# Kernel tuning notes

Hardware: AMD Instinct MI355X
Metric: run time of the kernel (lower is better)

## Reference

```python
import jax, jax.numpy as jnp
import numpy as np

LN_EPS = 1e-5
L1_EPS = 1e-12  # F.normalize clamp_min eps


def _layernorm(h, g, b):
    mu = h.mean(-1, keepdims=True)
    var = ((h - mu) ** 2).mean(-1, keepdims=True)
    return (h - mu) * jax.lax.rsqrt(var + LN_EPS) * g + b


def _graph(x, wq_w, wq_b, wk_w, wk_b, gcn_w, ln_g, ln_b):
    # x: [..., n, d]
    qx = x @ wq_w.T + wq_b
    kx = x @ wk_w.T + wk_b
    dot = jnp.einsum('...nd,...md->...nm', qx, kx)
    sq = dot * dot
    adj = sq / jnp.maximum(sq.sum(-1, keepdims=True), L1_EPS)  # L1-normalized rows
    for i in range(gcn_w.shape[0]):
        h = adj @ (x @ gcn_w[i])
        x = jax.nn.relu(_layernorm(h, ln_g[i], ln_b[i]))
    return x.mean(-2)  # mean over nodes -> [..., d]


def setup_inputs() -> dict:
    key = jax.random.key(0)
    ks = jax.random.split(key, 12)
    N, FR, B, NF = 16, 32, 50, 768
    L, NC = 2, 400
    s = 1.0 / np.sqrt(NF)
    inp = {
        'feats': jax.random.normal(ks[0], (N, FR, B, NF), jnp.float32),
        'feat_global_single': jax.random.normal(ks[1], (N, NF), jnp.float32),
        'feat_single_previous': jax.random.normal(ks[2], (N, NF), jnp.float32),
        'wq_w': jax.random.normal(ks[3], (NF, NF), jnp.float32) * s,
        'wq_b': jnp.zeros((NF,), jnp.float32),
        'wk_w': jax.random.normal(ks[4], (NF, NF), jnp.float32) * s,
        'wk_b': jnp.zeros((NF,), jnp.float32),
        'gcn_w': jax.random.normal(ks[5], (L, NF, NF), jnp.float32) * s,
        'ln_g': jnp.ones((L, NF), jnp.float32),
        'ln_b': jnp.zeros((L, NF), jnp.float32),
        'fc1_w': jax.random.normal(ks[6], (NF, 2 * NF), jnp.float32) / np.sqrt(2 * NF),
        'fc1_b': jnp.zeros((NF,), jnp.float32),
        'fc2_w': jax.random.normal(ks[7], (NC, NF), jnp.float32) * s,
        'fc2_b': jnp.zeros((NC,), jnp.float32),
        't_c': 0,
    }
    return inp


def reference(feats, feat_global_single, feat_single_previous,
              wq_w, wq_b, wk_w, wk_b, gcn_w, ln_g, ln_b,
              fc1_w, fc1_b, fc2_w, fc2_b, t_c):
    N, FR, B, NF = feats.shape
    x = feats.reshape(N * FR, B, NF)
    # object-level graph (shared weights)
    x = _graph(x, wq_w, wq_b, wk_w, wk_b, gcn_w, ln_g, ln_b)  # [N*FR, NF]
    x = x.reshape(N, FR, NF)
    # frame-level graph (same shared weights)
    x = _graph(x, wq_w, wq_b, wk_w, wk_b, gcn_w, ln_g, ln_b)  # [N, NF]
    y = jnp.concatenate([x, feat_global_single], axis=-1)      # [N, 2*NF]
    # ClassifierSimple (dropout = identity in eval)
    h = jax.nn.relu(y @ fc1_w.T + fc1_b)
    logits = h @ fc2_w.T + fc2_b
    return (logits, y)
```

## Files before the change

kernel.cpp:

```cpp
#include <hip/hip_runtime.h>
#include <hip/hip_bf16.h>

typedef unsigned short u16;
typedef unsigned int   u32;
typedef __attribute__((ext_vector_type(8))) short short8;
typedef __attribute__((ext_vector_type(4))) float float4v;

__device__ __forceinline__ float bf2f(u16 u){ union{u32 i; float f;} c; c.i = ((u32)u) << 16; return c.f; }
__device__ __forceinline__ float bflo(u32 u){ union{u32 i; float f;} c; c.i = u << 16; return c.f; }
__device__ __forceinline__ float bfhi(u32 u){ union{u32 i; float f;} c; c.i = u & 0xFFFF0000u; return c.f; }
__device__ __forceinline__ u16 f2bf(float f){
  union{float f; u32 i;} c; c.f = f; u32 x = c.i;
  return (u16)((x + 0x7FFFu + ((x >> 16) & 1u)) >> 16);
}
__device__ __forceinline__ u32 pack2(float a, float b){
  union { __hip_bfloat162 h; u32 u; } c;
  c.h = __float22bfloat162_rn(float2{a, b});
  return c.u;
}

__device__ __forceinline__ void async16(const void* g, void* l){
  __builtin_amdgcn_global_load_lds((const __attribute__((address_space(1))) void*)g,
                                   (__attribute__((address_space(3))) void*)l, 16, 0, 0);
}

__global__ void prep_w(const float* __restrict__ wq, const float* __restrict__ wk,
                       const float* __restrict__ gcn,
                       u16* __restrict__ WqT, u16* __restrict__ WkT,
                       u16* __restrict__ QHB768, u16* __restrict__ gcnT1)
{
  __shared__ float tile[32][33];
  int z = blockIdx.z;
  const float* src = (z == 0) ? wq : (z == 1) ? wk : gcn + (size_t)(z - 2) * 589824;
  u16* dst = (z == 0) ? WqT : (z == 1) ? WkT : (z == 2) ? QHB768 : gcnT1;
  int r0 = blockIdx.y * 32, c0 = blockIdx.x * 32;
  int tx = threadIdx.x, ty = threadIdx.y;
  for (int i = 0; i < 32; i += 8) tile[ty + i][tx] = src[(size_t)(r0 + ty + i) * 768 + c0 + tx];
  __syncthreads();
  for (int i = 0; i < 32; i += 8) dst[(size_t)(c0 + ty + i) * 768 + r0 + tx] = f2bf(tile[tx][ty + i]);
}

__global__ void __launch_bounds__(256) prep_uv2(const float* __restrict__ wq, const float* __restrict__ wk,
                                                const float* __restrict__ wqb, const float* __restrict__ wkb,
                                                float* __restrict__ uv, float* __restrict__ cbuf)
{
  __shared__ float red[4][64];
  __shared__ float r2[256];
  int b = blockIdx.x, tid = threadIdx.x;
  if (b < 24) {
    const float* w  = (b < 12) ? wq : wk;
    const float* bs = (b < 12) ? wkb : wqb;
    int out = (b % 12) * 64 + (tid & 63);
    int oq = tid >> 6;
    float a = 0.f;
    for (int o = oq * 192; o < oq * 192 + 192; o++) a += w[(size_t)o * 768 + out] * bs[o];
    red[oq][tid & 63] = a;
    __syncthreads();
    if (tid < 64)
      uv[((b < 12) ? 0 : 768) + (b % 12) * 64 + tid] = red[0][tid] + red[1][tid] + red[2][tid] + red[3][tid];
  } else {
    float a = 0.f;
    for (int o = tid; o < 768; o += 256) a += wqb[o] * wkb[o];
    r2[tid] = a; __syncthreads();
    if (tid == 0) { float s = 0.f; for (int i = 0; i < 256; i++) s += r2[i]; cbuf[0] = s; }
  }
}

__global__ void __launch_bounds__(256) conv_pq(const float* __restrict__ src, u16* __restrict__ dst,
                                               const float* __restrict__ uv, const float* __restrict__ cbuf,
                                               float* __restrict__ p, float* __restrict__ q)
{
  __shared__ float us[768], vs[768];
  int tid = threadIdx.x, lane = tid & 63;
  for (int i = tid; i < 768; i += 256) { us[i] = uv[i]; vs[i] = uv[768 + i]; }
  __syncthreads();
  size_t rbase = (size_t)blockIdx.x * 8;
  int row = tid >> 5;
  int c3  = (tid & 31) * 3;
  const float* s = src + (rbase + row) * 768 + (size_t)c3 * 8;
  u16* d = dst + (rbase + row) * 768 + (size_t)c3 * 8;
  float ap = 0.f, aq = 0.f;
#pragma unroll
  for (int j = 0; j < 3; j++) {
    float4 a = ((const float4*)s)[j * 2];
    float4 b = ((const float4*)s)[j * 2 + 1];
    uint4 o = { pack2(a.x, a.y), pack2(a.z, a.w), pack2(b.x, b.y), pack2(b.z, b.w) };
    ((uint4*)d)[j] = o;
    const float* uu = &us[(c3 + j) * 8];
    const float* vv = &vs[(c3 + j) * 8];
    ap += a.x*uu[0] + a.y*uu[1] + a.z*uu[2] + a.w*uu[3] + b.x*uu[4] + b.y*uu[5] + b.z*uu[6] + b.w*uu[7];
    aq += a.x*vv[0] + a.y*vv[1] + a.z*vv[2] + a.w*vv[3] + b.x*vv[4] + b.y*vv[5] + b.z*vv[6] + b.w*vv[7];
  }
  for (int m = 1; m <= 16; m <<= 1) { ap += __shfl_xor(ap, m); aq += __shfl_xor(aq, m); }
  if ((lane & 31) == 0) {
    p[rbase + row] = ap + cbuf[0];
    q[rbase + row] = aq;
  }
}

__global__ void __launch_bounds__(256) gemm_bt(const u16* __restrict__ A, const u16* __restrict__ Bw,
                                               const float* __restrict__ bias, u16* __restrict__ C,
                                               int M, int N, int K)
{
  __shared__ __attribute__((aligned(16))) u16 As[128 * 64];
  __shared__ __attribute__((aligned(16))) u16 Bs[128 * 64];
  int tid = threadIdx.x, lane = tid & 63, wid = tid >> 6;
  int wm = wid >> 1, wn = wid & 1;
  size_t m0 = (size_t)blockIdx.x * 128, n0 = (size_t)blockIdx.y * 128;

  float4v acc[4][4];
  for (int r = 0; r < 4; r++) for (int c = 0; c < 4; c++) acc[r][c] = (float4v){0.f, 0.f, 0.f, 0.f};

  int srow8  = lane >> 3;
  int schunk = (lane & 7) ^ srow8;
  const u16* gA[4]; const u16* gB[4];
  u16* lA[4]; u16* lB[4];
#pragma unroll
  for (int j = 0; j < 4; j++) {
    int r = 32 * wid + 8 * j + srow8;
    gA[j] = A  + (m0 + r) * (size_t)K + schunk * 8;
    gB[j] = Bw + (n0 + r) * (size_t)K + schunk * 8;
    lA[j] = &As[(32 * wid + 8 * j) * 64];
    lB[j] = &Bs[(32 * wid + 8 * j) * 64];
  }

  int l15 = lane & 15, quad = lane >> 4;
  int s0 = quad ^ (l15 & 7);

  for (int kt = 0; kt < K; kt += 64) {
#pragma unroll
    for (int j = 0; j < 4; j++) {
      async16(gA[j] + kt, lA[j]);
      async16(gB[j] + kt, lB[j]);
    }
    __syncthreads();
#pragma unroll
    for (int ks = 0; ks < 2; ks++) {
      int so = (s0 ^ (ks << 2)) * 8;
      short8 af[4], bfr[4];
#pragma unroll
      for (int r = 0; r < 4; r++) af[r]  = *(const short8*)&As[(wm * 64 + r * 16 + l15) * 64 + so];
#pragma unroll
      for (int c = 0; c < 4; c++) bfr[c] = *(const short8*)&Bs[(wn * 64 + c * 16 + l15) * 64 + so];
#pragma unroll
      for (int r = 0; r < 4; r++)
#pragma unroll
        for (int c = 0; c < 4; c++)
          acc[r][c] = __builtin_amdgcn_mfma_f32_16x16x32_bf16(af[r], bfr[c], acc[r][c], 0, 0, 0);
    }
    __syncthreads();
  }

  int quad4 = quad * 4;
  for (int c = 0; c < 4; c++) {
    int n = (int)n0 + wn * 64 + c * 16 + l15;
    float bv = bias ? bias[n] : 0.f;
    for (int r = 0; r < 4; r++) {
      size_t mbase = m0 + wm * 64 + r * 16 + quad4;
      for (int t = 0; t < 4; t++)
        C[(mbase + t) * (size_t)N + n] = f2bf(acc[r][c][t] + bv);
    }
  }
}


template<int NP>
__global__ void __launch_bounds__(512) fused_l1(const u16* __restrict__ TH, const u16* __restrict__ AR,
                                                const float* __restrict__ pb, const float* __restrict__ qb,
                                                const float* __restrict__ lng, const float* __restrict__ lnb,
                                                u16* __restrict__ adjG, u16* __restrict__ X, int n, int Mtot)
{
  constexpr int ST = 72;
  constexpr int TPW = (NP == 64) ? 2 : 1;
  constexpr int SR = NP;
  __shared__ __attribute__((aligned(16))) u16 adjb[NP * ST];
  __shared__ __attribute__((aligned(16))) u16 HT[2][64 * ST];
  __shared__ __attribute__((aligned(16))) u16 As1[SR * 64];
  __shared__ __attribute__((aligned(16))) u16 Bs1[SR * 64];
  __shared__ float rsum[NP];
  __shared__ float stats[NP][2];
  __shared__ float bc[NP][2];
  __shared__ float ps[NP], qs[NP];
  __shared__ float lg[768], lb[768];

  int g = blockIdx.x;
  int tid = threadIdx.x, lane = tid & 63, w = tid >> 6;
  int l15 = lane & 15, quad = lane >> 4;

  for (int i = tid; i < 768; i += 512) { lg[i] = lng[i]; lb[i] = lnb[i]; }
  if (tid < NP) {
    rsum[tid] = 0.f; stats[tid][0] = 0.f; stats[tid][1] = 0.f;
    ps[tid] = (tid < n) ? pb[(size_t)g * n + tid] : 0.f;
    qs[tid] = (tid < n) ? qb[(size_t)g * n + tid] : 0.f;
  }
  __syncthreads();

  int mt, nt0; bool s_act;
  if (NP == 64) { mt = w & 3; nt0 = (w >> 2) * 2; s_act = true; }
  else          { mt = w & 1; nt0 = w >> 1;       s_act = (w < 4); }

  int srow8  = lane >> 3;
  int schunk = (lane & 7) ^ srow8;
  int trow   = (NP == 64) ? (8 * w + srow8) : (8 * (w & 3) + srow8);
  size_t grow = (size_t)g * n + trow;
  if (grow >= (size_t)Mtot) grow = Mtot - 1;
  const u16* gA1 = TH + grow * 1536 + schunk * 8;
  const u16* gB1 = AR + grow * 768  + schunk * 8;
  u16* lA1 = &As1[((NP == 64) ? 8 * w : 8 * (w & 3)) * 64];
  u16* lB1 = &Bs1[((NP == 64) ? 8 * w : 8 * (w & 3)) * 64];
  int s0 = quad ^ (l15 & 7);

  float4v sacc[TPW];
  for (int j = 0; j < TPW; j++) sacc[j] = (float4v){0.f, 0.f, 0.f, 0.f};

  for (int kt = 0; kt < 768; kt += 64) {
    if (NP == 64) {
      async16(gA1 + kt, lA1);
      async16(gB1 + kt, lB1);
    } else {
      if (w < 4) async16(gA1 + kt, lA1);
      else       async16(gB1 + kt, lB1);
    }
    __syncthreads();
    if (s_act) {
#pragma unroll
      for (int ks = 0; ks < 2; ks++) {
        int so = (s0 ^ (ks << 2)) * 8;
        short8 a = *(const short8*)&As1[(mt * 16 + l15) * 64 + so];
#pragma unroll
        for (int j = 0; j < TPW; j++) {
          short8 b = *(const short8*)&Bs1[((nt0 + j) * 16 + l15) * 64 + so];
          sacc[j] = __builtin_amdgcn_mfma_f32_16x16x32_bf16(a, b, sacc[j], 0, 0, 0);
        }
      }
    }
    __syncthreads();
  }

  if (s_act) {
    for (int j = 0; j < TPW; j++) {
      int col = (nt0 + j) * 16 + l15;
      bool cok = col < n;
      for (int t = 0; t < 4; t++) {
        int row = mt * 16 + quad * 4 + t;
        sacc[j][t] = cok ? (sacc[j][t] + ps[row] + qs[col]) : 0.f;
      }
    }
    for (int t = 0; t < 4; t++) {
      float s = 0.f;
      for (int j = 0; j < TPW; j++) { float v = sacc[j][t]; s += v * v; }
      s += __shfl_xor(s, 1); s += __shfl_xor(s, 2); s += __shfl_xor(s, 4); s += __shfl_xor(s, 8);
      if (l15 == 0) atomicAdd(&rsum[mt * 16 + quad * 4 + t], s);
    }
  }
  __syncthreads();
  if (tid < NP) rsum[tid] = 1.0f / fmaxf(rsum[tid], 1e-12f);
  __syncthreads();
  if (s_act) {
    u16* gadj = adjG + (size_t)g * NP * NP;
    for (int j = 0; j < TPW; j++)
      for (int t = 0; t < 4; t++) {
        int row = mt * 16 + quad * 4 + t, col = (nt0 + j) * 16 + l15;
        float v = sacc[j][t];
        u16 b = f2bf(v * v * rsum[row]);
        adjb[row * ST + col] = b;
        gadj[row * NP + col] = b;
      }
  }
  __syncthreads();

  int m2, nt20;
  if (NP == 64) { m2 = w & 3; nt20 = (w >> 2) * 2; }
  else          { m2 = w & 1; nt20 = w >> 1; }

  float4v xacc[12][TPW];
#pragma unroll
  for (int ch = 0; ch < 12; ch++) for (int j = 0; j < TPW; j++) xacc[ch][j] = (float4v){0.f,0.f,0.f,0.f};

  int hj  = tid & (NP - 1);
  int hseg= (NP == 64) ? w : ((tid >> 5) & 7);
  bool hact = (NP == 64) ? true : (tid < NP * 8);
  const u16* hbase = TH + ((size_t)g * n + hj) * 1536 + 768 + hseg * 8;

  uint4 hcur = {0,0,0,0};
  if (hact && hj < n) hcur = *(const uint4*)(hbase);

#pragma unroll
  for (int ch = 0; ch < 12; ch++) {
    uint4 hnext = {0,0,0,0};
    if (ch < 11 && hact && hj < n) hnext = *(const uint4*)(hbase + (ch + 1) * 64);
    u16* htb = HT[ch & 1];
    if (hact) {
      const u16* ep = (const u16*)&hcur;
      for (int i = 0; i < 8; i++) htb[(hseg * 8 + i) * ST + hj] = ep[i];
    }
    __syncthreads();
    for (int k = 0; k < NP / 32; k++) {
      short8 a = *(const short8*)&adjb[(m2 * 16 + l15) * ST + k * 32 + quad * 8];
      for (int j = 0; j < TPW; j++) {
        short8 b = *(const short8*)&htb[((nt20 + j) * 16 + l15) * ST + k * 32 + quad * 8];
        xacc[ch][j] = __builtin_amdgcn_mfma_f32_16x16x32_bf16(a, b, xacc[ch][j], 0, 0, 0);
      }
    }
    hcur = hnext;
  }

  float ssum[4] = {0,0,0,0}, ssq[4] = {0,0,0,0};
#pragma unroll
  for (int ch = 0; ch < 12; ch++)
    for (int j = 0; j < TPW; j++)
      for (int t = 0; t < 4; t++) { float v = xacc[ch][j][t]; ssum[t] += v; ssq[t] += v * v; }
  for (int m = 1; m <= 8; m <<= 1)
    for (int t = 0; t < 4; t++) { ssum[t] += __shfl_xor(ssum[t], m); ssq[t] += __shfl_xor(ssq[t], m); }
  if (l15 == 0)
    for (int t = 0; t < 4; t++) {
      atomicAdd(&stats[m2 * 16 + quad * 4 + t][0], ssum[t]);
      atomicAdd(&stats[m2 * 16 + quad * 4 + t][1], ssq[t]);
    }
  __syncthreads();
  if (tid < NP) {
    float mu = stats[tid][0] * (1.f / 768.f);
    float var = stats[tid][1] * (1.f / 768.f) - mu * mu;
    bc[tid][0] = mu; bc[tid][1] = rsqrtf(fmaxf(var, 0.f) + 1e-5f);
  }
  __syncthreads();

#pragma unroll
  for (int ch = 0; ch < 12; ch++)
    for (int j = 0; j < TPW; j++)
      for (int t = 0; t < 4; t++) {
        int row = m2 * 16 + quad * 4 + t;
        if (row < n) {
          int d = ch * 64 + (nt20 + j) * 16 + l15;
          float v = fmaxf((xacc[ch][j][t] - bc[row][0]) * bc[row][1] * lg[d] + lb[d], 0.f);
          X[((size_t)g * n + row) * 768 + d] = f2bf(v);
        }
      }
}

template<int NP>
__global__ void __launch_bounds__(512) fused_l2(const u16* __restrict__ adjG, const u16* __restrict__ H,
                                                const float* __restrict__ lng, const float* __restrict__ lnb,
                                                u16* __restrict__ Xmean, int n, float inv,
                                                const float* __restrict__ uvg, const float* __restrict__ cbuf,
                                                float* __restrict__ pOut, float* __restrict__ qOut)
{
  constexpr int ST = 72;
  constexpr int TPW = (NP == 64) ? 2 : 1;
  __shared__ __attribute__((aligned(16))) u16 adjb[NP * ST];
  __shared__ __attribute__((aligned(16))) u16 HT[2][64 * ST];
  __shared__ float stats[NP][2];
  __shared__ float bc[NP][2];
  __shared__ float colsum[768];
  __shared__ float lg[768], lb[768];
  __shared__ float pr[8][2];

  int g = blockIdx.x;
  int tid = threadIdx.x, lane = tid & 63, w = tid >> 6;
  int l15 = lane & 15, quad = lane >> 4;

  for (int i = tid; i < 768; i += 512) { lg[i] = lng[i]; lb[i] = lnb[i]; colsum[i] = 0.f; }
  if (tid < NP) { stats[tid][0] = 0.f; stats[tid][1] = 0.f; }
  if (tid * 8 < NP * NP) {
    int row = (tid * 8) / NP, c0 = (tid * 8) % NP;
    uint4 v = *(const uint4*)(adjG + (size_t)g * NP * NP + row * NP + c0);
    *(uint4*)&adjb[row * ST + c0] = v;
  }

  int m2, nt20;
  if (NP == 64) { m2 = w & 3; nt20 = (w >> 2) * 2; }
  else          { m2 = w & 1; nt20 = w >> 1; }

  float4v xacc[12][TPW];
#pragma unroll
  for (int ch = 0; ch < 12; ch++) for (int j = 0; j < TPW; j++) xacc[ch][j] = (float4v){0.f,0.f,0.f,0.f};

  int hj  = tid & (NP - 1);
  int hseg= (NP == 64) ? w : ((tid >> 5) & 7);
  bool hact = (NP == 64) ? true : (tid < NP * 8);
  const u16* hbase = H + ((size_t)g * n + hj) * 768 + hseg * 8;

  uint4 hcur = {0,0,0,0};
  if (hact && hj < n) hcur = *(const uint4*)(hbase);

  __syncthreads();

#pragma unroll
  for (int ch = 0; ch < 12; ch++) {
    uint4 hnext = {0,0,0,0};
    if (ch < 11 && hact && hj < n) hnext = *(const uint4*)(hbase + (ch + 1) * 64);
    u16* htb = HT[ch & 1];
    if (hact) {
      const u16* ep = (const u16*)&hcur;
      for (int i = 0; i < 8; i++) htb[(hseg * 8 + i) * ST + hj] = ep[i];
    }
    __syncthreads();
    for (int k = 0; k < NP / 32; k++) {
      short8 a = *(const short8*)&adjb[(m2 * 16 + l15) * ST + k * 32 + quad * 8];
      for (int j = 0; j < TPW; j++) {
        short8 b = *(const short8*)&htb[((nt20 + j) * 16 + l15) * ST + k * 32 + quad * 8];
        xacc[ch][j] = __builtin_amdgcn_mfma_f32_16x16x32_bf16(a, b, xacc[ch][j], 0, 0, 0);
      }
    }
    hcur = hnext;
  }

  float ssum[4] = {0,0,0,0}, ssq[4] = {0,0,0,0};
#pragma unroll
  for (int ch = 0; ch < 12; ch++)
    for (int j = 0; j < TPW; j++)
      for (int t = 0; t < 4; t++) { float v = xacc[ch][j][t]; ssum[t] += v; ssq[t] += v * v; }
  for (int m = 1; m <= 8; m <<= 1)
    for (int t = 0; t < 4; t++) { ssum[t] += __shfl_xor(ssum[t], m); ssq[t] += __shfl_xor(ssq[t], m); }
  if (l15 == 0)
    for (int t = 0; t < 4; t++) {
      atomicAdd(&stats[m2 * 16 + quad * 4 + t][0], ssum[t]);
      atomicAdd(&stats[m2 * 16 + quad * 4 + t][1], ssq[t]);
    }
  __syncthreads();
  if (tid < NP) {
    float mu = stats[tid][0] * (1.f / 768.f);
    float var = stats[tid][1] * (1.f / 768.f) - mu * mu;
    bc[tid][0] = mu; bc[tid][1] = rsqrtf(fmaxf(var, 0.f) + 1e-5f);
  }
  __syncthreads();

#pragma unroll
  for (int ch = 0; ch < 12; ch++)
    for (int j = 0; j < TPW; j++)
      for (int t = 0; t < 4; t++) {
        int row = m2 * 16 + quad * 4 + t;
        int d = ch * 64 + (nt20 + j) * 16 + l15;
        float v = fmaxf((xacc[ch][j][t] - bc[row][0]) * bc[row][1] * lg[d] + lb[d], 0.f);
        float vm = (row < n) ? v : 0.f;
        vm += __shfl_xor(vm, 16);
        vm += __shfl_xor(vm, 32);
        if (quad == 0) atomicAdd(&colsum[d], vm);
      }
  __syncthreads();
  if (tid < 384)
    ((u32*)Xmean)[(size_t)g * 384 + tid] = pack2(colsum[tid * 2] * inv, colsum[tid * 2 + 1] * inv);

  if (pOut) {
    float pp = 0.f, qq = 0.f;
    if (tid < 384) {
      float x0 = colsum[tid * 2] * inv, x1 = colsum[tid * 2 + 1] * inv;
      pp = x0 * uvg[tid * 2] + x1 * uvg[tid * 2 + 1];
      qq = x0 * uvg[768 + tid * 2] + x1 * uvg[768 + tid * 2 + 1];
    }
    for (int m = 1; m <= 32; m <<= 1) { pp += __shfl_xor(pp, m); qq += __shfl_xor(qq, m); }
    if (lane == 0) { pr[w][0] = pp; pr[w][1] = qq; }
    __syncthreads();
    if (tid == 0) {
      float sp = 0.f, sq = 0.f;
      for (int i = 0; i < 8; i++) { sp += pr[i][0]; sq += pr[i][1]; }
      pOut[g] = sp + cbuf[0]; qOut[g] = sq;
    }
  }
}

__global__ void __launch_bounds__(384) concat_y(const u16* __restrict__ Xm,
                                                const float* __restrict__ fgs, float* __restrict__ yout)
{
  int b = blockIdx.x, tid = threadIdx.x;
  u32 u = ((const u32*)Xm)[(size_t)b * 384 + tid];
  int d0 = tid * 2;
  yout[(size_t)b * 1536 + d0]     = bflo(u);
  yout[(size_t)b * 1536 + d0 + 1] = bfhi(u);
  yout[(size_t)b * 1536 + 768 + d0]     = fgs[(size_t)b * 768 + d0];
  yout[(size_t)b * 1536 + 768 + d0 + 1] = fgs[(size_t)b * 768 + d0 + 1];
}

__global__ void __launch_bounds__(256) fc1_relu(const float* __restrict__ yout,
                                                const float* __restrict__ fc1w, const float* __restrict__ fc1b,
                                                float* __restrict__ h)
{
  int o = blockIdx.x * 4 + (threadIdx.x >> 6);
  int lane = threadIdx.x & 63;
  float acc[16];
  for (int b = 0; b < 16; b++) acc[b] = 0.f;
  const float4* wr = (const float4*)(fc1w + (size_t)o * 1536);
  for (int k4 = lane; k4 < 384; k4 += 64) {
    float4 wv = wr[k4];
    for (int b = 0; b < 16; b++) {
      float4 yv = ((const float4*)(yout + (size_t)b * 1536))[k4];
      acc[b] += wv.x * yv.x + wv.y * yv.y + wv.z * yv.z + wv.w * yv.w;
    }
  }
  for (int m = 1; m <= 32; m <<= 1)
    for (int b = 0; b < 16; b++) acc[b] += __shfl_xor(acc[b], m);
  if (lane < 16) h[(size_t)lane * 768 + o] = fmaxf(acc[lane] + fc1b[o], 0.f);
}

__global__ void __launch_bounds__(256) fc2_out(const float* __restrict__ h,
                                               const float* __restrict__ fc2w, const float* __restrict__ fc2b,
                                               float* __restrict__ logits)
{
  int o = blockIdx.x * 4 + (threadIdx.x >> 6);
  int lane = threadIdx.x & 63;
  float acc[16];
  for (int b = 0; b < 16; b++) acc[b] = 0.f;
  const float4* wr = (const float4*)(fc2w + (size_t)o * 768);
  for (int k4 = lane; k4 < 192; k4 += 64) {
    float4 wv = wr[k4];
    for (int b = 0; b < 16; b++) {
      float4 hv = ((const float4*)(h + (size_t)b * 768))[k4];
      acc[b] += wv.x * hv.x + wv.y * hv.y + wv.z * hv.z + wv.w * hv.w;
    }
  }
  for (int m = 1; m <= 32; m <<= 1)
    for (int b = 0; b < 16; b++) acc[b] += __shfl_xor(acc[b], m);
  if (lane < 16) logits[(size_t)lane * 400 + o] = acc[lane] + fc2b[o];
}

extern "C" void kernel_launch(void* const* d_in, const int* in_sizes, int n_in,
                              void* d_out, int out_size, void* d_ws, size_t ws_size,
                              hipStream_t stream) {
  const float* feats = (const float*)d_in[0];
  const float* fgs   = (const float*)d_in[1];
  const float* wq_w  = (const float*)d_in[3];
  const float* wq_b  = (const float*)d_in[4];
  const float* wk_w  = (const float*)d_in[5];
  const float* wk_b  = (const float*)d_in[6];
  const float* gcn_w = (const float*)d_in[7];
  const float* ln_g  = (const float*)d_in[8];
  const float* ln_b  = (const float*)d_in[9];
  const float* fc1_w = (const float*)d_in[10];
  const float* fc1_b = (const float*)d_in[11];
  const float* fc2_w = (const float*)d_in[12];
  const float* fc2_b = (const float*)d_in[13];
  float* out  = (float*)d_out;
  float* yout = out + 16 * 400;

  char* ws = (char*)d_ws;
  size_t off = 0;
  auto alloc = [&](size_t b){ size_t r = off; off = (off + b + 255) & ~(size_t)255; return r; };
  u16*  QHB    = (u16*) (ws + alloc((size_t)1536 * 768 * 2));
  u16*  gcnT1  = (u16*) (ws + alloc((size_t)768 * 768 * 2));
  u16*  WqT    = (u16*) (ws + alloc((size_t)768 * 768 * 2));
  u16*  WkT    = (u16*) (ws + alloc((size_t)768 * 768 * 2));
  float* uv    = (float*)(ws + alloc((size_t)1536 * 4));
  float* cbuf  = (float*)(ws + alloc((size_t)4));
  u16*  Abf    = (u16*) (ws + alloc((size_t)25600 * 768 * 2));
  float* pObj  = (float*)(ws + alloc((size_t)25600 * 4));
  float* qObj  = (float*)(ws + alloc((size_t)25600 * 4));
  float* pF    = (float*)(ws + alloc((size_t)512 * 4));
  float* qF    = (float*)(ws + alloc((size_t)512 * 4));
  u16*  Xf     = (u16*) (ws + alloc((size_t)512 * 768 * 2));
  u16*  QHf    = (u16*) (ws + alloc((size_t)512 * 1536 * 2));
  u16*  X1f    = (u16*) (ws + alloc((size_t)512 * 768 * 2));
  u16*  H2f    = (u16*) (ws + alloc((size_t)512 * 768 * 2));
  u16*  adjFb  = (u16*) (ws + alloc((size_t)16 * 32 * 32 * 2));
  u16*  Xm     = (u16*) (ws + alloc((size_t)16 * 768 * 2));
  float* hbuf  = (float*)(ws + alloc((size_t)16 * 768 * 4));
  size_t base = off;

  auto need = [&](int GC){
    size_t R = (size_t)GC * 50;
    return base + R * 1536 * 2 + 512 + R * 768 * 2 + 512 + (size_t)GC * 64 * 64 * 2 + 512;
  };
  int GC = 64;
  if (need(512) <= ws_size) GC = 512;
  else if (need(256) <= ws_size) GC = 256;
  else if (need(128) <= ws_size) GC = 128;
  int R = GC * 50;
  size_t off2 = base;
  auto alloc2 = [&](size_t b){ size_t r = off2; off2 = (off2 + b + 255) & ~(size_t)255; return r; };
  u16* QHc   = (u16*)(ws + alloc2((size_t)R * 1536 * 2));
  u16* X1c   = (u16*)(ws + alloc2((size_t)R * 768 * 2));
  u16* adjGc = (u16*)(ws + alloc2((size_t)GC * 64 * 64 * 2));
  u16* H2c   = QHc;

  prep_w<<<dim3(24, 24, 4), dim3(32, 8), 0, stream>>>(wq_w, wk_w, gcn_w, WqT, WkT,
                                                      QHB + (size_t)768 * 768, gcnT1);
  prep_uv2<<<25, 256, 0, stream>>>(wq_w, wk_w, wq_b, wk_b, uv, cbuf);
  gemm_bt<<<dim3(6, 6), 256, 0, stream>>>(WkT, WqT, nullptr, QHB, 768, 768, 768);
  conv_pq<<<3200, 256, 0, stream>>>(feats, Abf, uv, cbuf, pObj, qObj);

  int nchunks = 512 / GC;
  for (int c = 0; c < nchunks; c++) {
    const u16* fc = Abf + (size_t)c * GC * 50 * 768;
    gemm_bt<<<dim3(R / 128, 12), 256, 0, stream>>>(fc, QHB, nullptr, QHc, R, 1536, 768);
    fused_l1<64><<<GC, 512, 0, stream>>>(QHc, fc, pObj + (size_t)c * GC * 50, qObj + (size_t)c * GC * 50,
                                         ln_g, ln_b, adjGc, X1c, 50, R);
    gemm_bt<<<dim3(R / 128, 6), 256, 0, stream>>>(X1c, gcnT1, nullptr, H2c, R, 768, 768);
    fused_l2<64><<<GC, 512, 0, stream>>>(adjGc, H2c, ln_g + 768, ln_b + 768,
                                         Xf + (size_t)c * GC * 768, 50, 1.f / 50.f,
                                         uv, cbuf, pF + (size_t)c * GC, qF + (size_t)c * GC);
  }

  gemm_bt<<<dim3(4, 12), 256, 0, stream>>>(Xf, QHB, nullptr, QHf, 512, 1536, 768);
  fused_l1<32><<<16, 512, 0, stream>>>(QHf, Xf, pF, qF, ln_g, ln_b, adjFb, X1f, 32, 512);
  gemm_bt<<<dim3(4, 6), 256, 0, stream>>>(X1f, gcnT1, nullptr, H2f, 512, 768, 768);
  fused_l2<32><<<16, 512, 0, stream>>>(adjFb, H2f, ln_g + 768, ln_b + 768, Xm, 32, 1.f / 32.f,
                                       uv, cbuf, nullptr, nullptr);

  concat_y<<<16, 384, 0, stream>>>(Xm, fgs, yout);
  fc1_relu<<<192, 256, 0, stream>>>(yout, fc1_w, fc1_b, hbuf);
  fc2_out<<<100, 256, 0, stream>>>(hbuf, fc2_w, fc2_b, out);
}
```

Before: 494.8 us.

## Produce transposed H via swapped GEMM operands and load with swizzled vector LDS stores

The combined QH GEMM is split into two calls. One keeps the row-major T output. The other swaps operands so that H1 and H2 are written transposed (feature-major, leading dimension R). The fused graph kernels then load H with 16-byte vector LDS stores into an XOR-swizzled layout, replacing the 8-way scalar transposing scatter and removing the per-row bounds checks. Padding and a zero_tail kernel cover reads past the last group. In exchange, the transposed GEMM has a different output write pattern and there is an extra launch, and rows read past n pick up neighbouring groups' data, which must be masked by zero adjacency.

```diff
diff --git a/kernel.cpp b/kernel.cpp
--- a/kernel.cpp
+++ b/kernel.cpp
@@ -66,6 +66,12 @@
   }
 }
 
+__global__ void zero_tail(u16* a, u16* b, u16* c, u16* d)
+{
+  int t = threadIdx.x;
+  a[t] = 0; b[t] = 0; c[t] = 0; d[t] = 0;
+}
+
 __global__ void __launch_bounds__(256) conv_pq(const float* __restrict__ src, u16* __restrict__ dst,
                                                const float* __restrict__ uv, const float* __restrict__ cbuf,
                                                float* __restrict__ p, float* __restrict__ q)
@@ -165,18 +171,19 @@
 
 
 template<int NP>
-__global__ void __launch_bounds__(512) fused_l1(const u16* __restrict__ TH, const u16* __restrict__ AR,
+__global__ void __launch_bounds__(512) fused_l1(const u16* __restrict__ Tc, const u16* __restrict__ AR,
                                                 const float* __restrict__ pb, const float* __restrict__ qb,
                                                 const float* __restrict__ lng, const float* __restrict__ lnb,
-                                                u16* __restrict__ adjG, u16* __restrict__ X, int n, int Mtot)
+                                                u16* __restrict__ adjG, u16* __restrict__ X, int n, int Mtot,
+                                                const u16* __restrict__ HTg, int ldH)
 {
   constexpr int ST = 72;
   constexpr int TPW = (NP == 64) ? 2 : 1;
-  constexpr int SR = NP;
+  constexpr int NOCT = NP / 8;
   __shared__ __attribute__((aligned(16))) u16 adjb[NP * ST];
-  __shared__ __attribute__((aligned(16))) u16 HT[2][64 * ST];
-  __shared__ __attribute__((aligned(16))) u16 As1[SR * 64];
-  __shared__ __attribute__((aligned(16))) u16 Bs1[SR * 64];
+  __shared__ __attribute__((aligned(16))) u16 HT[2][64 * NP];
+  __shared__ __attribute__((aligned(16))) u16 As1[NP * 64];
+  __shared__ __attribute__((aligned(16))) u16 Bs1[NP * 64];
   __shared__ float rsum[NP];
   __shared__ float stats[NP][2];
   __shared__ float bc[NP][2];
@@ -204,8 +211,8 @@
   int trow   = (NP == 64) ? (8 * w + srow8) : (8 * (w & 3) + srow8);
   size_t grow = (size_t)g * n + trow;
   if (grow >= (size_t)Mtot) grow = Mtot - 1;
-  const u16* gA1 = TH + grow * 1536 + schunk * 8;
-  const u16* gB1 = AR + grow * 768  + schunk * 8;
+  const u16* gA1 = Tc + grow * 768 + schunk * 8;
+  const u16* gB1 = AR + grow * 768 + schunk * 8;
   u16* lA1 = &As1[((NP == 64) ? 8 * w : 8 * (w & 3)) * 64];
   u16* lB1 = &Bs1[((NP == 64) ? 8 * w : 8 * (w & 3)) * 64];
   int s0 = quad ^ (l15 & 7);
@@ -277,28 +284,28 @@
 #pragma unroll
   for (int ch = 0; ch < 12; ch++) for (int j = 0; j < TPW; j++) xacc[ch][j] = (float4v){0.f,0.f,0.f,0.f};
 
-  int hj  = tid & (NP - 1);
-  int hseg= (NP == 64) ? w : ((tid >> 5) & 7);
-  bool hact = (NP == 64) ? true : (tid < NP * 8);
-  const u16* hbase = TH + ((size_t)g * n + hj) * 1536 + 768 + hseg * 8;
+  int dloc = tid / NOCT;
+  int oct  = tid % NOCT;
+  bool hact = tid < 64 * NOCT;
+  int hslot = oct ^ (dloc & (NOCT - 1));
+  const u16* hbase = HTg + (size_t)dloc * ldH + (size_t)g * n + oct * 8;
 
   uint4 hcur = {0,0,0,0};
-  if (hact && hj < n) hcur = *(const uint4*)(hbase);
+  if (hact) hcur = *(const uint4*)(hbase);
 
 #pragma unroll
   for (int ch = 0; ch < 12; ch++) {
     uint4 hnext = {0,0,0,0};
-    if (ch < 11 && hact && hj < n) hnext = *(const uint4*)(hbase + (ch + 1) * 64);
+    if (ch < 11 && hact) hnext = *(const uint4*)(hbase + (size_t)(ch + 1) * 64 * ldH);
     u16* htb = HT[ch & 1];
-    if (hact) {
-      const u16* ep = (const u16*)&hcur;
-      for (int i = 0; i < 8; i++) htb[(hseg * 8 + i) * ST + hj] = ep[i];
-    }
+    if (hact) *(uint4*)&htb[dloc * NP + hslot * 8] = hcur;
     __syncthreads();
     for (int k = 0; k < NP / 32; k++) {
       short8 a = *(const short8*)&adjb[(m2 * 16 + l15) * ST + k * 32 + quad * 8];
       for (int j = 0; j < TPW; j++) {
-        short8 b = *(const short8*)&htb[((nt20 + j) * 16 + l15) * ST + k * 32 + quad * 8];
+        int drow = (nt20 + j) * 16 + l15;
+        int rs = ((k * 4 + quad) ^ (l15 & (NOCT - 1))) * 8;
+        short8 b = *(const short8*)&htb[drow * NP + rs];
         xacc[ch][j] = __builtin_amdgcn_mfma_f32_16x16x32_bf16(a, b, xacc[ch][j], 0, 0, 0);
       }
     }
@@ -339,7 +346,8 @@
 }
 
 template<int NP>
-__global__ void __launch_bounds__(512) fused_l2(const u16* __restrict__ adjG, const u16* __restrict__ H,
+__global__ void __launch_bounds__(512) fused_l2(const u16* __restrict__ adjG, const u16* __restrict__ HTg,
+                                                int ldH,
                                                 const float* __restrict__ lng, const float* __restrict__ lnb,
                                                 u16* __restrict__ Xmean, int n, float inv,
                                                 const float* __restrict__ uvg, const float* __restrict__ cbuf,
@@ -347,8 +355,9 @@
 {
   constexpr int ST = 72;
   constexpr int TPW = (NP == 64) ? 2 : 1;
+  constexpr int NOCT = NP / 8;
   __shared__ __attribute__((aligned(16))) u16 adjb[NP * ST];
-  __shared__ __attribute__((aligned(16))) u16 HT[2][64 * ST];
+  __shared__ __attribute__((aligned(16))) u16 HT[2][64 * NP];
   __shared__ float stats[NP][2];
   __shared__ float bc[NP][2];
   __shared__ float colsum[768];
@@ -375,30 +384,30 @@
 #pragma unroll
   for (int ch = 0; ch < 12; ch++) for (int j = 0; j < TPW; j++) xacc[ch][j] = (float4v){0.f,0.f,0.f,0.f};
 
-  int hj  = tid & (NP - 1);
-  int hseg= (NP == 64) ? w : ((tid >> 5) & 7);
-  bool hact = (NP == 64) ? true : (tid < NP * 8);
-  const u16* hbase = H + ((size_t)g * n + hj) * 768 + hseg * 8;
+  int dloc = tid / NOCT;
+  int oct  = tid % NOCT;
+  bool hact = tid < 64 * NOCT;
+  int hslot = oct ^ (dloc & (NOCT - 1));
+  const u16* hbase = HTg + (size_t)dloc * ldH + (size_t)g * n + oct * 8;
 
   uint4 hcur = {0,0,0,0};
-  if (hact && hj < n) hcur = *(const uint4*)(hbase);
+  if (hact) hcur = *(const uint4*)(hbase);
 
   __syncthreads();
 
 #pragma unroll
   for (int ch = 0; ch < 12; ch++) {
     uint4 hnext = {0,0,0,0};
-    if (ch < 11 && hact && hj < n) hnext = *(const uint4*)(hbase + (ch + 1) * 64);
+    if (ch < 11 && hact) hnext = *(const uint4*)(hbase + (size_t)(ch + 1) * 64 * ldH);
     u16* htb = HT[ch & 1];
-    if (hact) {
-      const u16* ep = (const u16*)&hcur;
-      for (int i = 0; i < 8; i++) htb[(hseg * 8 + i) * ST + hj] = ep[i];
-    }
+    if (hact) *(uint4*)&htb[dloc * NP + hslot * 8] = hcur;
     __syncthreads();
     for (int k = 0; k < NP / 32; k++) {
       short8 a = *(const short8*)&adjb[(m2 * 16 + l15) * ST + k * 32 + quad * 8];
       for (int j = 0; j < TPW; j++) {
-        short8 b = *(const short8*)&htb[((nt20 + j) * 16 + l15) * ST + k * 32 + quad * 8];
+        int drow = (nt20 + j) * 16 + l15;
+        int rs = ((k * 4 + quad) ^ (l15 & (NOCT - 1))) * 8;
+        short8 b = *(const short8*)&htb[drow * NP + rs];
         xacc[ch][j] = __builtin_amdgcn_mfma_f32_16x16x32_bf16(a, b, xacc[ch][j], 0, 0, 0);
       }
     }
@@ -547,9 +556,9 @@
   float* pF    = (float*)(ws + alloc((size_t)512 * 4));
   float* qF    = (float*)(ws + alloc((size_t)512 * 4));
   u16*  Xf     = (u16*) (ws + alloc((size_t)512 * 768 * 2));
-  u16*  QHf    = (u16*) (ws + alloc((size_t)512 * 1536 * 2));
+  u16*  QHf    = (u16*) (ws + alloc((size_t)512 * 1536 * 2 + 256));
   u16*  X1f    = (u16*) (ws + alloc((size_t)512 * 768 * 2));
-  u16*  H2f    = (u16*) (ws + alloc((size_t)512 * 768 * 2));
+  u16*  H2f    = (u16*) (ws + alloc((size_t)512 * 768 * 2 + 256));
   u16*  adjFb  = (u16*) (ws + alloc((size_t)16 * 32 * 32 * 2));
   u16*  Xm     = (u16*) (ws + alloc((size_t)16 * 768 * 2));
   float* hbuf  = (float*)(ws + alloc((size_t)16 * 768 * 4));
@@ -557,7 +566,8 @@
 
   auto need = [&](int GC){
     size_t R = (size_t)GC * 50;
-    return base + R * 1536 * 2 + 512 + R * 768 * 2 + 512 + (size_t)GC * 64 * 64 * 2 + 512;
+    return base + (R * 768 * 2 + 256) + 512 + (768 * R * 2 + 256) + 512
+                + R * 768 * 2 + 512 + (size_t)GC * 64 * 64 * 2 + 512;
   };
   int GC = 64;
   if (need(512) <= ws_size) GC = 512;
@@ -566,33 +576,42 @@
   int R = GC * 50;
   size_t off2 = base;
   auto alloc2 = [&](size_t b){ size_t r = off2; off2 = (off2 + b + 255) & ~(size_t)255; return r; };
-  u16* QHc   = (u16*)(ws + alloc2((size_t)R * 1536 * 2));
+  u16* Tc    = (u16*)(ws + alloc2((size_t)R * 768 * 2 + 256));
+  u16* H1T   = (u16*)(ws + alloc2((size_t)768 * R * 2 + 256));
   u16* X1c   = (u16*)(ws + alloc2((size_t)R * 768 * 2));
   u16* adjGc = (u16*)(ws + alloc2((size_t)GC * 64 * 64 * 2));
-  u16* H2c   = QHc;
+  u16* H2T   = Tc;
+
+  u16* Tf    = QHf;
+  u16* H1Tf  = QHf + (size_t)512 * 768;
+  u16* H2Tf  = H2f;
 
   prep_w<<<dim3(24, 24, 4), dim3(32, 8), 0, stream>>>(wq_w, wk_w, gcn_w, WqT, WkT,
                                                       QHB + (size_t)768 * 768, gcnT1);
   prep_uv2<<<25, 256, 0, stream>>>(wq_w, wk_w, wq_b, wk_b, uv, cbuf);
   gemm_bt<<<dim3(6, 6), 256, 0, stream>>>(WkT, WqT, nullptr, QHB, 768, 768, 768);
   conv_pq<<<3200, 256, 0, stream>>>(feats, Abf, uv, cbuf, pObj, qObj);
+  zero_tail<<<1, 64, 0, stream>>>(H1T + (size_t)768 * R, Tc + (size_t)768 * R,
+                                  H1Tf + (size_t)768 * 512, H2Tf + (size_t)768 * 512);
 
   int nchunks = 512 / GC;
   for (int c = 0; c < nchunks; c++) {
     const u16* fc = Abf + (size_t)c * GC * 50 * 768;
-    gemm_bt<<<dim3(R / 128, 12), 256, 0, stream>>>(fc, QHB, nullptr, QHc, R, 1536, 768);
-    fused_l1<64><<<GC, 512, 0, stream>>>(QHc, fc, pObj + (size_t)c * GC * 50, qObj + (size_t)c * GC * 50,
-                                         ln_g, ln_b, adjGc, X1c, 50, R);
-    gemm_bt<<<dim3(R / 128, 6), 256, 0, stream>>>(X1c, gcnT1, nullptr, H2c, R, 768, 768);
-    fused_l2<64><<<GC, 512, 0, stream>>>(adjGc, H2c, ln_g + 768, ln_b + 768,
+    gemm_bt<<<dim3(R / 128, 6), 256, 0, stream>>>(fc, QHB, nullptr, Tc, R, 768, 768);
+    gemm_bt<<<dim3(6, R / 128), 256, 0, stream>>>(QHB + (size_t)768 * 768, fc, nullptr, H1T, 768, R, 768);
+    fused_l1<64><<<GC, 512, 0, stream>>>(Tc, fc, pObj + (size_t)c * GC * 50, qObj + (size_t)c * GC * 50,
+                                         ln_g, ln_b, adjGc, X1c, 50, R, H1T, R);
+    gemm_bt<<<dim3(6, R / 128), 256, 0, stream>>>(gcnT1, X1c, nullptr, H2T, 768, R, 768);
+    fused_l2<64><<<GC, 512, 0, stream>>>(adjGc, H2T, R, ln_g + 768, ln_b + 768,
                                          Xf + (size_t)c * GC * 768, 50, 1.f / 50.f,
                                          uv, cbuf, pF + (size_t)c * GC, qF + (size_t)c * GC);
   }
 
-  gemm_bt<<<dim3(4, 12), 256, 0, stream>>>(Xf, QHB, nullptr, QHf, 512, 1536, 768);
-  fused_l1<32><<<16, 512, 0, stream>>>(QHf, Xf, pF, qF, ln_g, ln_b, adjFb, X1f, 32, 512);
-  gemm_bt<<<dim3(4, 6), 256, 0, stream>>>(X1f, gcnT1, nullptr, H2f, 512, 768, 768);
-  fused_l2<32><<<16, 512, 0, stream>>>(adjFb, H2f, ln_g + 768, ln_b + 768, Xm, 32, 1.f / 32.f,
+  gemm_bt<<<dim3(4, 6), 256, 0, stream>>>(Xf, QHB, nullptr, Tf, 512, 768, 768);
+  gemm_bt<<<dim3(6, 4), 256, 0, stream>>>(QHB + (size_t)768 * 768, Xf, nullptr, H1Tf, 768, 512, 768);
+  fused_l1<32><<<16, 512, 0, stream>>>(Tf, Xf, pF, qF, ln_g, ln_b, adjFb, X1f, 32, 512, H1Tf, 512);
+  gemm_bt<<<dim3(6, 4), 256, 0, stream>>>(gcnT1, X1f, nullptr, H2Tf, 768, 512, 768);
+  fused_l2<32><<<16, 512, 0, stream>>>(adjFb, H2Tf, 512, ln_g + 768, ln_b + 768, Xm, 32, 1.f / 32.f,
                                        uv, cbuf, nullptr, nullptr);
 
   concat_y<<<16, 384, 0, stream>>>(Xm, fgs, yout);
```

Result: slower. 556.2 us (+12.4%).
